# Performance work log

Measured on AMD Instinct MI355X. Metric: run time of the kernel, lower is better.

The kernel has to match this reference:

```python
import jax, jax.numpy as jnp
import numpy as np

V, E, H, L, B, T = 32000, 256, 512, 2, 64, 2048


def setup_inputs() -> dict:
    key = jax.random.key(0)
    ks = jax.random.split(key, 24)
    def rn(i, shape, scale=0.05):
        return jax.random.normal(ks[i], shape, jnp.float32) * scale
    inp = {
        "token": jax.random.randint(ks[0], (B,), 0, V),
        "h0": rn(1, (L, B, H), 1.0),
        "c0": rn(2, (L, B, H), 1.0),
        "encoder_outputs": rn(3, (B, T, H), 1.0),
        "mask": jax.random.randint(ks[4], (B, T), 0, 2).astype(jnp.int32),
        # parameters
        "emb_table": rn(5, (V, E), 1.0).at[0].set(0.0),  # padding_idx=0
        "W_attn": rn(6, (H, 2 * H)),
        "b_attn": rn(7, (H,)),
        "v_attn": jax.random.uniform(ks[8], (H,), jnp.float32),  # torch.rand init
        "W_ih0": rn(9, (4 * H, E + H)),
        "W_hh0": rn(10, (4 * H, H)),
        "b_ih0": rn(11, (4 * H,)),
        "b_hh0": rn(12, (4 * H,)),
        "W_ih1": rn(13, (4 * H, H)),
        "W_hh1": rn(14, (4 * H, H)),
        "b_ih1": rn(15, (4 * H,)),
        "b_hh1": rn(16, (4 * H,)),
        "W_out": rn(17, (V, H)),
        "b_out": rn(18, (V,)),
    }
    return inp


def _lstm_step(x, h, c, Wi, Wh, bi, bh):
    # PyTorch gate order: i, f, g, o
    gates = x @ Wi.T + bi + h @ Wh.T + bh  # [B, 4H]
    i, f, g, o = jnp.split(gates, 4, axis=-1)
    c_new = jax.nn.sigmoid(f) * c + jax.nn.sigmoid(i) * jnp.tanh(g)
    h_new = jax.nn.sigmoid(o) * jnp.tanh(c_new)
    return h_new, c_new


def reference(token, h0, c0, encoder_outputs, mask,
              emb_table, W_attn, b_attn, v_attn,
              W_ih0, W_hh0, b_ih0, b_hh0,
              W_ih1, W_hh1, b_ih1, b_hh1,
              W_out, b_out):
    embedded = emb_table[token]  # [B, E]

    # Bahdanau attention using the top-layer hidden state.
    # Linear on concat(hidden, enc) split into two matmuls (no T-tiling of hidden).
    h_top = h0[-1]  # [B, H]
    h_part = h_top @ W_attn[:, :H].T  # [B, H]
    e_part = jnp.einsum('bth,kh->btk', encoder_outputs, W_attn[:, H:])  # [B, T, H]
    energy = jnp.tanh(h_part[:, None, :] + e_part + b_attn) @ v_attn  # [B, T]
    energy = jnp.where(mask == 0, -jnp.inf, energy)
    attn_weights = jax.nn.softmax(energy, axis=1)  # [B, T]

    context = jnp.einsum('bt,bth->bh', attn_weights, encoder_outputs)  # [B, H]

    # Single-step 2-layer LSTM (eval mode: no inter-layer dropout).
    x0 = jnp.concatenate([embedded, context], axis=-1)  # [B, E+H]
    h0_new, c0_new = _lstm_step(x0, h0[0], c0[0], W_ih0, W_hh0, b_ih0, b_hh0)
    h1_new, c1_new = _lstm_step(h0_new, h0[1], c0[1], W_ih1, W_hh1, b_ih1, b_hh1)

    logits = h1_new @ W_out.T + b_out  # [B, V]
    h_new = jnp.stack([h0_new, h1_new])  # [L, B, H]
    c_new = jnp.stack([c0_new, c1_new])
    return logits, (h_new, c_new), attn_weights
```

## Files before the change

### kernel.cpp

```cpp
#include <hip/hip_runtime.h>
#include <hip/hip_fp16.h>
#include <cmath>

typedef _Float16 f16x8 __attribute__((ext_vector_type(8)));
typedef _Float16 f16x4 __attribute__((ext_vector_type(4)));
typedef float f32x4 __attribute__((ext_vector_type(4)));

#define NV 32000
#define NE 256
#define NH 512
#define NB 64
#define NT 2048

__device__ __forceinline__ float fast_tanh(float x) {
  return 1.f - 2.f / (__expf(2.f * x) + 1.f);
}
__device__ __forceinline__ float fast_sig(float x) {
  return 1.f / (1.f + __expf(-x));
}

__global__ void k_swz_be(const float* __restrict__ Wattn, _Float16* __restrict__ Be) {
  int idx = blockIdx.x * 256 + threadIdx.x;
  int l = idx & 63, nt = (idx >> 6) & 31, kc = idx >> 11;
  int n = (nt << 4) + (l & 15);
  int h0 = (kc << 5) + ((l >> 4) << 3);
  const float* s = Wattn + n * 1024 + 512 + h0;
  _Float16* d = Be + idx * 8;
  #pragma unroll
  for (int j = 0; j < 8; ++j) d[j] = (_Float16)s[j];
}

__global__ void k_prep_htop(const float* __restrict__ h0, _Float16* __restrict__ xh,
                            _Float16* __restrict__ xcat1) {
  int b = blockIdx.x, t = threadIdx.x;
  _Float16 v = (_Float16)h0[NB * NH + b * NH + t];
  xh[b * NH + t] = v;
  xcat1[b * 1024 + 512 + t] = v;
}

template <int KLEN>
__global__ __launch_bounds__(128)
void k_gemm_bT(const _Float16* __restrict__ A, int K,
               const float* __restrict__ B0, int ldb0,
               const float* __restrict__ B1, int ldb1, int b1k,
               const float* __restrict__ bias,
               float* __restrict__ out, int N) {
  int ntiles = N >> 5;
  int bn = blockIdx.x % ntiles, kcid = blockIdx.x / ntiles;
  int tid = threadIdx.x, w = tid >> 6, l = tid & 63;
  int n = (bn << 5) + (w << 4) + (l & 15);
  int kq = (l >> 4) << 3;
  int k0 = kcid * KLEN;
  f32x4 acc[4];
  #pragma unroll
  for (int mi = 0; mi < 4; ++mi) acc[mi] = (f32x4){0.f, 0.f, 0.f, 0.f};
  #pragma unroll 2
  for (int kk = 0; kk < KLEN; kk += 32) {
    int kbase = k0 + kk;
    f16x8 a[4];
    #pragma unroll
    for (int mi = 0; mi < 4; ++mi)
      a[mi] = *(const f16x8*)(A + (size_t)((l & 15) + (mi << 4)) * K + kbase + kq);
    const float* bp;
    if (B1 && kbase >= b1k) bp = B1 + (size_t)n * ldb1 + (kbase - b1k) + kq;
    else                    bp = B0 + (size_t)n * ldb0 + kbase + kq;
    float4 x0 = *(const float4*)bp;
    float4 x1 = *(const float4*)(bp + 4);
    f16x8 bf = {(_Float16)x0.x, (_Float16)x0.y, (_Float16)x0.z, (_Float16)x0.w,
                (_Float16)x1.x, (_Float16)x1.y, (_Float16)x1.z, (_Float16)x1.w};
    #pragma unroll
    for (int mi = 0; mi < 4; ++mi)
      acc[mi] = __builtin_amdgcn_mfma_f32_16x16x32_f16(a[mi], bf, acc[mi], 0, 0, 0);
  }
  float* op = out + (size_t)kcid * 64 * N;
  #pragma unroll
  for (int mi = 0; mi < 4; ++mi)
    #pragma unroll
    for (int r = 0; r < 4; ++r) {
      int row = (mi << 4) + ((l >> 4) << 2) + r;
      float v = acc[mi][r];
      if (bias) v += bias[n];
      op[(size_t)row * N + n] = v;
    }
}

__global__ __launch_bounds__(512, 4)
void k_energy(const float* __restrict__ enc, const _Float16* __restrict__ Be,
              const float* __restrict__ hp0, const float* __restrict__ hp1,
              const float* __restrict__ battn, const float* __restrict__ vat,
              const int* __restrict__ mask,
              float* __restrict__ eng, float* __restrict__ mcsc,
              float* __restrict__ numpart) {
  __shared__ _Float16 As[64 * 512];
  __shared__ float hpl[NH], vl[NH], ep[64][8], wl[64];
  int tile = blockIdx.x;
  int b = tile >> 5;
  long row0 = (long)tile << 6;
  int tid = threadIdx.x;
  hpl[tid] = hp0[(b << 9) + tid] + hp1[(b << 9) + tid] + battn[tid];
  vl[tid] = vat[tid];
  int w = tid >> 6, l = tid & 63;

  const float4* encp = (const float4*)(enc + row0 * NH);
  for (int half = 0; half < 2; ++half) {
    float4 st[8];
    #pragma unroll
    for (int i = 0; i < 8; ++i) st[i] = encp[tid + ((half * 8 + i) << 9)];
    #pragma unroll
    for (int i = 0; i < 8; ++i) {
      int s = tid + ((half * 8 + i) << 9);
      int r = s >> 7, c4 = s & 127;
      f16x4 h4 = {(_Float16)st[i].x, (_Float16)st[i].y,
                  (_Float16)st[i].z, (_Float16)st[i].w};
      *(f16x4*)((char*)As + (r << 10) + (((c4 << 3)) ^ ((r & 7) << 4))) = h4;
    }
  }
  __syncthreads();

  f32x4 acc[4][4];
  #pragma unroll
  for (int mi = 0; mi < 4; ++mi)
    #pragma unroll
    for (int ni = 0; ni < 4; ++ni) acc[mi][ni] = (f32x4){0.f, 0.f, 0.f, 0.f};

  for (int kc = 0; kc < 16; ++kc) {
    f16x8 a[4], bf[4];
    int kb = (kc << 6) + ((l >> 4) << 4);
    #pragma unroll
    for (int mi = 0; mi < 4; ++mi) {
      int r = (mi << 4) + (l & 15);
      a[mi] = *(const f16x8*)((char*)As + (r << 10) + (kb ^ ((r & 7) << 4)));
    }
    #pragma unroll
    for (int ni = 0; ni < 4; ++ni)
      bf[ni] = *(const f16x8*)(Be + (size_t)((((kc << 5) + (w << 2) + ni) << 6) + l) * 8);
    #pragma unroll
    for (int mi = 0; mi < 4; ++mi)
      #pragma unroll
      for (int ni = 0; ni < 4; ++ni)
        acc[mi][ni] = __builtin_amdgcn_mfma_f32_16x16x32_f16(a[mi], bf[ni], acc[mi][ni], 0, 0, 0);
  }

  int cl = l & 15;
  #pragma unroll
  for (int mi = 0; mi < 4; ++mi) {
    float s0 = 0.f, s1 = 0.f, s2 = 0.f, s3 = 0.f;
    #pragma unroll
    for (int ni = 0; ni < 4; ++ni) {
      int col = (w << 6) + (ni << 4) + cl;
      float hv = hpl[col], vv = vl[col];
      s0 += vv * fast_tanh(acc[mi][ni][0] + hv);
      s1 += vv * fast_tanh(acc[mi][ni][1] + hv);
      s2 += vv * fast_tanh(acc[mi][ni][2] + hv);
      s3 += vv * fast_tanh(acc[mi][ni][3] + hv);
    }
    #pragma unroll
    for (int off = 1; off < 16; off <<= 1) {
      s0 += __shfl_xor(s0, off, 64);
      s1 += __shfl_xor(s1, off, 64);
      s2 += __shfl_xor(s2, off, 64);
      s3 += __shfl_xor(s3, off, 64);
    }
    if (cl == 0) {
      int rb = (mi << 4) + ((l >> 4) << 2);
      ep[rb][w] = s0; ep[rb + 1][w] = s1; ep[rb + 2][w] = s2; ep[rb + 3][w] = s3;
    }
  }
  __syncthreads();

  if (tid < 64) {
    float e = 0.f;
    #pragma unroll
    for (int q = 0; q < 8; ++q) e += ep[tid][q];
    int mk = mask[row0 + tid];
    e = mk ? e : -3.0e38f;
    eng[row0 + tid] = e;
    float m = e;
    #pragma unroll
    for (int off = 32; off; off >>= 1) m = fmaxf(m, __shfl_xor(m, off, 64));
    float wv = mk ? __expf(e - m) : 0.f;
    float s = wv;
    #pragma unroll
    for (int off = 32; off; off >>= 1) s += __shfl_xor(s, off, 64);
    wl[tid] = wv;
    if (tid == 0) { mcsc[tile * 2] = m; mcsc[tile * 2 + 1] = s; }
  }
  __syncthreads();

  float a = 0.f;
  #pragma unroll 4
  for (int t = 0; t < 64; ++t) {
    float ev = (float)(*(const _Float16*)((char*)As + (t << 10) + (((tid * 2)) ^ ((t & 7) << 4))));
    a += wl[t] * ev;
  }
  numpart[(size_t)tile * NH + tid] = a;
}

__global__ void k_combine(const float* __restrict__ mcsc, const float* __restrict__ numpart,
                          const float* __restrict__ eng, const int* __restrict__ token,
                          const float* __restrict__ emb, const float* __restrict__ h0,
                          _Float16* __restrict__ xcat0, float* __restrict__ attw) {
  __shared__ float scale_s[32], Ms, dens;
  int b = blockIdx.x, tid = threadIdx.x;
  if (tid < 32) {
    float m = mcsc[(b * 32 + tid) * 2];
    float s = mcsc[(b * 32 + tid) * 2 + 1];
    float M = m;
    #pragma unroll
    for (int off = 16; off; off >>= 1) M = fmaxf(M, __shfl_xor(M, off, 32));
    float sc = __expf(m - M);
    float d = sc * s;
    #pragma unroll
    for (int off = 16; off; off >>= 1) d += __shfl_xor(d, off, 32);
    scale_s[tid] = sc;
    if (tid == 0) { Ms = M; dens = d; }
  }
  __syncthreads();
  float M = Ms, rden = 1.f / dens;
  float a = 0.f;
  #pragma unroll 4
  for (int c = 0; c < 32; ++c) a += scale_s[c] * numpart[(size_t)(b * 32 + c) * NH + tid];
  xcat0[b * 1280 + 256 + tid] = (_Float16)(a * rden);
  if (tid < 256) xcat0[b * 1280 + tid] = (_Float16)emb[(size_t)token[b] * NE + tid];
  xcat0[b * 1280 + 768 + tid] = (_Float16)h0[b * NH + tid];
  #pragma unroll
  for (int i = 0; i < 4; ++i) {
    int t = tid + (i << 9);
    attw[(b << 11) + t] = __expf(eng[(b << 11) + t] - M) * rden;
  }
}

__global__ void k_act(const float* __restrict__ pg, const float* __restrict__ bih,
                      const float* __restrict__ bhh, const float* __restrict__ cprev,
                      float* __restrict__ hout, float* __restrict__ cout,
                      _Float16* __restrict__ hf16, int hpitch, int nchunks) {
  int idx = blockIdx.x * 256 + threadIdx.x;
  int b = idx >> 9, u = idx & 511;
  float g[4];
  #pragma unroll
  for (int gi = 0; gi < 4; ++gi) {
    float s = bih[gi * 512 + u] + bhh[gi * 512 + u];
    for (int kc = 0; kc < nchunks; ++kc)
      s += pg[((size_t)kc * 64 + b) * 2048 + gi * 512 + u];
    g[gi] = s;
  }
  float c = fast_sig(g[1]) * cprev[idx] + fast_sig(g[0]) * fast_tanh(g[2]);
  float h = fast_sig(g[3]) * fast_tanh(c);
  cout[idx] = c;
  hout[idx] = h;
  hf16[b * hpitch + u] = (_Float16)h;
}

extern "C" void kernel_launch(void* const* d_in, const int* in_sizes, int n_in,
                              void* d_out, int out_size, void* d_ws, size_t ws_size,
                              hipStream_t stream) {
  (void)in_sizes; (void)n_in; (void)out_size; (void)ws_size;
  const int*   token = (const int*)d_in[0];
  const float* h0    = (const float*)d_in[1];
  const float* c0    = (const float*)d_in[2];
  const float* enc   = (const float*)d_in[3];
  const int*   mask  = (const int*)d_in[4];
  const float* emb   = (const float*)d_in[5];
  const float* Wattn = (const float*)d_in[6];
  const float* battn = (const float*)d_in[7];
  const float* vattn = (const float*)d_in[8];
  const float* Wih0  = (const float*)d_in[9];
  const float* Whh0  = (const float*)d_in[10];
  const float* bih0  = (const float*)d_in[11];
  const float* bhh0  = (const float*)d_in[12];
  const float* Wih1  = (const float*)d_in[13];
  const float* Whh1  = (const float*)d_in[14];
  const float* bih1  = (const float*)d_in[15];
  const float* bhh1  = (const float*)d_in[16];
  const float* Wout  = (const float*)d_in[17];
  const float* bout  = (const float*)d_in[18];

  float* ws    = (float*)d_ws;
  float* pghp  = ws;
  float* eng   = pghp + 65536;
  float* mcsc  = eng + 131072;
  float* np    = mcsc + 4096;
  float* pg0   = np + 1048576;
  float* pg1   = pg0 + 524288;
  _Float16* Be    = (_Float16*)(pg1 + 524288);
  _Float16* xh    = Be + 262144;
  _Float16* xcat0 = xh + 32768;
  _Float16* xcat1 = xcat0 + 81920;
  _Float16* h1f   = xcat1 + 65536;

  float* out    = (float*)d_out;
  float* logits = out;
  float* hnew   = out + (size_t)NB * NV;
  float* cnew   = hnew + 2 * NB * NH;
  float* attw   = cnew + 2 * NB * NH;

  k_swz_be<<<dim3(128), dim3(256), 0, stream>>>(Wattn, Be);
  k_prep_htop<<<dim3(64), dim3(512), 0, stream>>>(h0, xh, xcat1);
  k_gemm_bT<256><<<dim3(32), dim3(128), 0, stream>>>(
      xh, NH, Wattn, 1024, nullptr, 0, 1 << 30, nullptr, pghp, NH);
  k_energy<<<dim3(2048), dim3(512), 0, stream>>>(
      enc, Be, pghp, pghp + 32768, battn, vattn, mask, eng, mcsc, np);
  k_combine<<<dim3(64), dim3(512), 0, stream>>>(
      mcsc, np, eng, token, emb, h0, xcat0, attw);
  k_gemm_bT<320><<<dim3(256), dim3(128), 0, stream>>>(
      xcat0, 1280, Wih0, 768, Whh0, NH, 768, nullptr, pg0, 2048);
  k_act<<<dim3(128), dim3(256), 0, stream>>>(
      pg0, bih0, bhh0, c0, hnew, cnew, xcat1, 1024, 4);
  k_gemm_bT<256><<<dim3(256), dim3(128), 0, stream>>>(
      xcat1, 1024, Wih1, NH, Whh1, NH, NH, nullptr, pg1, 2048);
  k_act<<<dim3(128), dim3(256), 0, stream>>>(
      pg1, bih1, bhh1, c0 + NB * NH, hnew + NB * NH, cnew + NB * NH, h1f, 512, 4);
  k_gemm_bT<512><<<dim3(1000), dim3(128), 0, stream>>>(
      h1f, NH, Wout, NH, nullptr, 0, 1 << 30, bout, logits, NV);
}
```

Before: 193.6 us.

## Overlap second-half encoder load with first-half MFMA and vectorize context reduction

The encoder tile is now staged into LDS in two K-halves. The global loads for the second half are issued before the first-half MFMA loop runs, so their latency is hidden behind compute. The per-tile softmax is computed redundantly by every wave, which drops one block barrier. The weighted context sum now reads f16x4 vectors across four row groups and combines them through a small LDS scratch buffer. This adds LDS usage and an extra reduction step, and the eight in-flight float4 registers per thread could raise register pressure.

```diff
diff --git a/kernel.cpp b/kernel.cpp
--- a/kernel.cpp
+++ b/kernel.cpp
@@ -84,6 +84,45 @@
     }
 }
 
+
+#define ISSUE8(rs, t, h)                                                       \
+  { const float4* gp = (const float4*)(enc + (size_t)(t) * 32768 + (h) * 256); \
+    _Pragma("unroll")                                                          \
+    for (int ii = 0; ii < 8; ++ii) {                                           \
+      int s_ = tid + ii * 512;                                                 \
+      rs[ii] = gp[(s_ >> 6) * 128 + (s_ & 63)];                                \
+    } }
+
+#define WRITE8(rs, h)                                                          \
+  { _Pragma("unroll")                                                          \
+    for (int ii = 0; ii < 8; ++ii) {                                           \
+      int s_ = tid + ii * 512;                                                 \
+      int r_ = s_ >> 6, c4_ = s_ & 63;                                         \
+      f16x4 h4_ = {(_Float16)rs[ii].x, (_Float16)rs[ii].y,                     \
+                   (_Float16)rs[ii].z, (_Float16)rs[ii].w};                    \
+      *(f16x4*)((char*)As + (r_ << 10) +                                       \
+                ((((h) << 9) + (c4_ << 3)) ^ ((r_ & 7) << 4))) = h4_;          \
+    } }
+
+#define MFMA_KC(klo, khi)                                                      \
+  for (int kc = (klo); kc < (khi); ++kc) {                                     \
+    f16x8 afr[4];                                                              \
+    _Pragma("unroll")                                                          \
+    for (int mi = 0; mi < 4; ++mi) {                                           \
+      int r_ = (mi << 4) + (l & 15);                                           \
+      afr[mi] = *(const f16x8*)((char*)As + (r_ << 10) +                       \
+                 (((kc << 6) + ((l >> 4) << 4)) ^ ((r_ & 7) << 4)));           \
+    }                                                                          \
+    _Pragma("unroll")                                                          \
+    for (int ni = 0; ni < 4; ++ni) {                                           \
+      f16x8 bfr = *(const f16x8*)(Be +                                         \
+          (size_t)((((kc << 5) + (w << 2) + ni) << 6) + l) * 8);               \
+      _Pragma("unroll")                                                        \
+      for (int mi = 0; mi < 4; ++mi)                                           \
+        acc[mi][ni] = __builtin_amdgcn_mfma_f32_16x16x32_f16(afr[mi], bfr,     \
+                                                             acc[mi][ni], 0, 0, 0); \
+    } }
+
 __global__ __launch_bounds__(512, 4)
 void k_energy(const float* __restrict__ enc, const _Float16* __restrict__ Be,
               const float* __restrict__ hp0, const float* __restrict__ hp1,
@@ -92,30 +131,18 @@
               float* __restrict__ eng, float* __restrict__ mcsc,
               float* __restrict__ numpart) {
   __shared__ _Float16 As[64 * 512];
-  __shared__ float hpl[NH], vl[NH], ep[64][8], wl[64];
+  __shared__ float hpl[NH], vl[NH], ep[64][8], wl[64], psc[4][NH];
   int tile = blockIdx.x;
   int b = tile >> 5;
   long row0 = (long)tile << 6;
-  int tid = threadIdx.x;
+  int tid = threadIdx.x, w = tid >> 6, l = tid & 63;
   hpl[tid] = hp0[(b << 9) + tid] + hp1[(b << 9) + tid] + battn[tid];
   vl[tid] = vat[tid];
-  int w = tid >> 6, l = tid & 63;
-
-  const float4* encp = (const float4*)(enc + row0 * NH);
-  for (int half = 0; half < 2; ++half) {
-    float4 st[8];
-    #pragma unroll
-    for (int i = 0; i < 8; ++i) st[i] = encp[tid + ((half * 8 + i) << 9)];
-    #pragma unroll
-    for (int i = 0; i < 8; ++i) {
-      int s = tid + ((half * 8 + i) << 9);
-      int r = s >> 7, c4 = s & 127;
-      f16x4 h4 = {(_Float16)st[i].x, (_Float16)st[i].y,
-                  (_Float16)st[i].z, (_Float16)st[i].w};
-      *(f16x4*)((char*)As + (r << 10) + (((c4 << 3)) ^ ((r & 7) << 4))) = h4;
-    }
-  }
-  __syncthreads();
+
+  float4 rs[8];
+  ISSUE8(rs, tile, 0);
+  WRITE8(rs, 0);
+  ISSUE8(rs, tile, 1);
 
   f32x4 acc[4][4];
   #pragma unroll
@@ -123,23 +150,11 @@
     #pragma unroll
     for (int ni = 0; ni < 4; ++ni) acc[mi][ni] = (f32x4){0.f, 0.f, 0.f, 0.f};
 
-  for (int kc = 0; kc < 16; ++kc) {
-    f16x8 a[4], bf[4];
-    int kb = (kc << 6) + ((l >> 4) << 4);
-    #pragma unroll
-    for (int mi = 0; mi < 4; ++mi) {
-      int r = (mi << 4) + (l & 15);
-      a[mi] = *(const f16x8*)((char*)As + (r << 10) + (kb ^ ((r & 7) << 4)));
-    }
-    #pragma unroll
-    for (int ni = 0; ni < 4; ++ni)
-      bf[ni] = *(const f16x8*)(Be + (size_t)((((kc << 5) + (w << 2) + ni) << 6) + l) * 8);
-    #pragma unroll
-    for (int mi = 0; mi < 4; ++mi)
-      #pragma unroll
-      for (int ni = 0; ni < 4; ++ni)
-        acc[mi][ni] = __builtin_amdgcn_mfma_f32_16x16x32_f16(a[mi], bf[ni], acc[mi][ni], 0, 0, 0);
-  }
+  __syncthreads();
+  MFMA_KC(0, 8);
+  WRITE8(rs, 1);
+  __syncthreads();
+  MFMA_KC(8, 16);
 
   int cl = l & 15;
   #pragma unroll
@@ -168,13 +183,13 @@
   }
   __syncthreads();
 
-  if (tid < 64) {
-    float e = 0.f;
-    #pragma unroll
-    for (int q = 0; q < 8; ++q) e += ep[tid][q];
-    int mk = mask[row0 + tid];
+  {
+    float4 e0 = *(const float4*)&ep[l][0];
+    float4 e1 = *(const float4*)&ep[l][4];
+    float e = (e0.x + e0.y) + (e0.z + e0.w) + (e1.x + e1.y) + (e1.z + e1.w);
+    int mk = mask[row0 + l];
     e = mk ? e : -3.0e38f;
-    eng[row0 + tid] = e;
+    if (w == 0) eng[row0 + l] = e;
     float m = e;
     #pragma unroll
     for (int off = 32; off; off >>= 1) m = fmaxf(m, __shfl_xor(m, off, 64));
@@ -182,18 +197,28 @@
     float s = wv;
     #pragma unroll
     for (int off = 32; off; off >>= 1) s += __shfl_xor(s, off, 64);
-    wl[tid] = wv;
+    wl[l] = wv;
     if (tid == 0) { mcsc[tile * 2] = m; mcsc[tile * 2 + 1] = s; }
   }
-  __syncthreads();
-
-  float a = 0.f;
-  #pragma unroll 4
-  for (int t = 0; t < 64; ++t) {
-    float ev = (float)(*(const _Float16*)((char*)As + (t << 10) + (((tid * 2)) ^ ((t & 7) << 4))));
-    a += wl[t] * ev;
-  }
-  numpart[(size_t)tile * NH + tid] = a;
+
+  {
+    int rg = tid >> 7, j4 = tid & 127;
+    float c0a = 0.f, c1a = 0.f, c2a = 0.f, c3a = 0.f;
+    #pragma unroll 4
+    for (int r16 = 0; r16 < 16; ++r16) {
+      int t = (rg << 4) + r16;
+      f16x4 hv = *(const f16x4*)((char*)As + (t << 10) +
+                                 ((j4 << 3) ^ ((t & 7) << 4)));
+      float wv = wl[t];
+      c0a += wv * (float)hv[0]; c1a += wv * (float)hv[1];
+      c2a += wv * (float)hv[2]; c3a += wv * (float)hv[3];
+    }
+    *(float4*)&psc[rg][j4 << 2] = (float4){c0a, c1a, c2a, c3a};
+  }
+  __syncthreads();
+
+  numpart[(size_t)tile * NH + tid] =
+      psc[0][tid] + psc[1][tid] + psc[2][tid] + psc[3][tid];
 }
 
 __global__ void k_combine(const float* __restrict__ mcsc, const float* __restrict__ numpart,
```

New measurement: 254.8 us. +31.6%, slower.

## Pipeline encoder loads into LDS asynchronously in a multi-tile energy kernel

Applied to the files above, without the earlier changes.

The energy kernel is restructured so each block handles 8 consecutive 64-row tiles rather than one, with the grid shrunk to 256 blocks. Encoder rows are streamed as fp32 straight into a 4-stage LDS ring via global_load_lds, using explicit vmcnt waits and barriers. Conversion to fp16 now happens while MFMA fragments are built, so global-memory latency overlaps with matrix work instead of sitting in a load-then-compute phase. The weighted context sum now re-reads the encoder tile from global memory (hoping for cache hits) instead of reusing an fp16 LDS copy. This raises LDS usage to about 140KB per block, which limits occupancy to one block per CU.

```diff
diff --git a/kernel.cpp b/kernel.cpp
--- a/kernel.cpp
+++ b/kernel.cpp
@@ -17,6 +17,10 @@
 }
 __device__ __forceinline__ float fast_sig(float x) {
   return 1.f / (1.f + __expf(-x));
+}
+__device__ __forceinline__ void gll16(const void* g, void* l) {
+  __builtin_amdgcn_global_load_lds((const __attribute__((address_space(1))) void*)g,
+                                   (__attribute__((address_space(3))) void*)l, 16, 0, 0);
 }
 
 __global__ void k_swz_be(const float* __restrict__ Wattn, _Float16* __restrict__ Be) {
@@ -84,116 +88,156 @@
     }
 }
 
-__global__ __launch_bounds__(512, 4)
+
+#define WAITVM(N) asm volatile("s_waitcnt vmcnt(" #N ")" ::: "memory")
+#define SBAR() { __builtin_amdgcn_sched_barrier(0); __builtin_amdgcn_s_barrier(); \
+                 __builtin_amdgcn_sched_barrier(0); }
+#define LBAR() { asm volatile("s_waitcnt lgkmcnt(0)" ::: "memory"); \
+                 __builtin_amdgcn_s_barrier(); __builtin_amdgcn_sched_barrier(0); }
+
+#define ISSUE(g)                                                               \
+  { int t_ = t0 + ((g) >> 2); int q_ = (g) & 3; float* bq_ = buf[q_];          \
+    _Pragma("unroll")                                                          \
+    for (int k_ = 0; k_ < 4; ++k_) {                                           \
+      int rw_ = (w << 3) + (k_ << 1) + (l >> 5);                               \
+      const char* gp_ = (const char*)enc + ((size_t)((t_ << 6) + rw_) << 11) + \
+                        (q_ << 9) + (((l & 31) << 4) ^ ((rw_ & 7) << 4));      \
+      gll16(gp_, (char*)&bq_[((w << 3) + (k_ << 1)) << 7]);                    \
+    } }
+
+__global__ __launch_bounds__(512, 2)
 void k_energy(const float* __restrict__ enc, const _Float16* __restrict__ Be,
               const float* __restrict__ hp0, const float* __restrict__ hp1,
               const float* __restrict__ battn, const float* __restrict__ vat,
               const int* __restrict__ mask,
               float* __restrict__ eng, float* __restrict__ mcsc,
               float* __restrict__ numpart) {
-  __shared__ _Float16 As[64 * 512];
-  __shared__ float hpl[NH], vl[NH], ep[64][8], wl[64];
-  int tile = blockIdx.x;
-  int b = tile >> 5;
-  long row0 = (long)tile << 6;
-  int tid = threadIdx.x;
+  __shared__ float buf[4][64 * 128];
+  __shared__ float hpl[NH], vl[NH], ep[64][8], wl[64], psc[4][NH];
+  __shared__ int ml[512];
+  int bid = blockIdx.x;
+  int tid = threadIdx.x, w = tid >> 6, l = tid & 63;
+  int b = bid >> 2;
+  int t0 = bid << 3;
+
   hpl[tid] = hp0[(b << 9) + tid] + hp1[(b << 9) + tid] + battn[tid];
   vl[tid] = vat[tid];
-  int w = tid >> 6, l = tid & 63;
-
-  const float4* encp = (const float4*)(enc + row0 * NH);
-  for (int half = 0; half < 2; ++half) {
-    float4 st[8];
-    #pragma unroll
-    for (int i = 0; i < 8; ++i) st[i] = encp[tid + ((half * 8 + i) << 9)];
-    #pragma unroll
-    for (int i = 0; i < 8; ++i) {
-      int s = tid + ((half * 8 + i) << 9);
-      int r = s >> 7, c4 = s & 127;
-      f16x4 h4 = {(_Float16)st[i].x, (_Float16)st[i].y,
-                  (_Float16)st[i].z, (_Float16)st[i].w};
-      *(f16x4*)((char*)As + (r << 10) + (((c4 << 3)) ^ ((r & 7) << 4))) = h4;
-    }
-  }
-  __syncthreads();
-
-  f32x4 acc[4][4];
-  #pragma unroll
-  for (int mi = 0; mi < 4; ++mi)
-    #pragma unroll
-    for (int ni = 0; ni < 4; ++ni) acc[mi][ni] = (f32x4){0.f, 0.f, 0.f, 0.f};
-
-  for (int kc = 0; kc < 16; ++kc) {
-    f16x8 a[4], bf[4];
-    int kb = (kc << 6) + ((l >> 4) << 4);
+  ml[tid] = mask[((size_t)t0 << 6) + tid];
+
+  ISSUE(0); ISSUE(1); ISSUE(2);
+
+  for (int j = 0; j < 8; ++j) {
+    int tile = t0 + j;
+    long row0 = (long)tile << 6;
+    f32x4 acc[4][4];
+    #pragma unroll
+    for (int mi = 0; mi < 4; ++mi)
+      #pragma unroll
+      for (int ni = 0; ni < 4; ++ni) acc[mi][ni] = (f32x4){0.f, 0.f, 0.f, 0.f};
+
+    for (int q = 0; q < 4; ++q) {
+      int g = (j << 2) + q;
+      if (g + 3 < 32) { ISSUE(g + 3); }
+      int rem = 31 - g;
+      if (rem >= 3)      WAITVM(12);
+      else if (rem == 2) WAITVM(8);
+      else if (rem == 1) WAITVM(4);
+      else               WAITVM(0);
+      LBAR();
+
+      const float* bq = buf[q];
+      #pragma unroll
+      for (int kcl = 0; kcl < 4; ++kcl) {
+        int kcg = (q << 2) + kcl;
+        f16x8 afr[4];
+        #pragma unroll
+        for (int mi = 0; mi < 4; ++mi) {
+          int r_ = (mi << 4) + (l & 15);
+          const char* rowp = (const char*)(bq + (r_ << 7));
+          int b0 = (kcl << 7) + ((l >> 4) << 5);
+          int sw = (r_ & 7) << 4;
+          f32x4 lo = *(const f32x4*)(rowp + (b0 ^ sw));
+          f32x4 hi = *(const f32x4*)(rowp + ((b0 + 16) ^ sw));
+          afr[mi] = (f16x8){(_Float16)lo[0], (_Float16)lo[1],
+                            (_Float16)lo[2], (_Float16)lo[3],
+                            (_Float16)hi[0], (_Float16)hi[1],
+                            (_Float16)hi[2], (_Float16)hi[3]};
+        }
+        #pragma unroll
+        for (int ni = 0; ni < 4; ++ni) {
+          f16x8 bfr = *(const f16x8*)(Be +
+              (size_t)((((kcg << 5) + (w << 2) + ni) << 6) + l) * 8);
+          #pragma unroll
+          for (int mi = 0; mi < 4; ++mi)
+            acc[mi][ni] = __builtin_amdgcn_mfma_f32_16x16x32_f16(
+                afr[mi], bfr, acc[mi][ni], 0, 0, 0);
+        }
+      }
+      SBAR();
+    }
+
+    int cl = l & 15;
     #pragma unroll
     for (int mi = 0; mi < 4; ++mi) {
-      int r = (mi << 4) + (l & 15);
-      a[mi] = *(const f16x8*)((char*)As + (r << 10) + (kb ^ ((r & 7) << 4)));
-    }
-    #pragma unroll
-    for (int ni = 0; ni < 4; ++ni)
-      bf[ni] = *(const f16x8*)(Be + (size_t)((((kc << 5) + (w << 2) + ni) << 6) + l) * 8);
-    #pragma unroll
-    for (int mi = 0; mi < 4; ++mi)
-      #pragma unroll
-      for (int ni = 0; ni < 4; ++ni)
-        acc[mi][ni] = __builtin_amdgcn_mfma_f32_16x16x32_f16(a[mi], bf[ni], acc[mi][ni], 0, 0, 0);
-  }
-
-  int cl = l & 15;
-  #pragma unroll
-  for (int mi = 0; mi < 4; ++mi) {
-    float s0 = 0.f, s1 = 0.f, s2 = 0.f, s3 = 0.f;
-    #pragma unroll
-    for (int ni = 0; ni < 4; ++ni) {
-      int col = (w << 6) + (ni << 4) + cl;
-      float hv = hpl[col], vv = vl[col];
-      s0 += vv * fast_tanh(acc[mi][ni][0] + hv);
-      s1 += vv * fast_tanh(acc[mi][ni][1] + hv);
-      s2 += vv * fast_tanh(acc[mi][ni][2] + hv);
-      s3 += vv * fast_tanh(acc[mi][ni][3] + hv);
-    }
-    #pragma unroll
-    for (int off = 1; off < 16; off <<= 1) {
-      s0 += __shfl_xor(s0, off, 64);
-      s1 += __shfl_xor(s1, off, 64);
-      s2 += __shfl_xor(s2, off, 64);
-      s3 += __shfl_xor(s3, off, 64);
-    }
-    if (cl == 0) {
-      int rb = (mi << 4) + ((l >> 4) << 2);
-      ep[rb][w] = s0; ep[rb + 1][w] = s1; ep[rb + 2][w] = s2; ep[rb + 3][w] = s3;
-    }
-  }
-  __syncthreads();
-
-  if (tid < 64) {
-    float e = 0.f;
-    #pragma unroll
-    for (int q = 0; q < 8; ++q) e += ep[tid][q];
-    int mk = mask[row0 + tid];
-    e = mk ? e : -3.0e38f;
-    eng[row0 + tid] = e;
-    float m = e;
-    #pragma unroll
-    for (int off = 32; off; off >>= 1) m = fmaxf(m, __shfl_xor(m, off, 64));
-    float wv = mk ? __expf(e - m) : 0.f;
-    float s = wv;
-    #pragma unroll
-    for (int off = 32; off; off >>= 1) s += __shfl_xor(s, off, 64);
-    wl[tid] = wv;
-    if (tid == 0) { mcsc[tile * 2] = m; mcsc[tile * 2 + 1] = s; }
-  }
-  __syncthreads();
-
-  float a = 0.f;
-  #pragma unroll 4
-  for (int t = 0; t < 64; ++t) {
-    float ev = (float)(*(const _Float16*)((char*)As + (t << 10) + (((tid * 2)) ^ ((t & 7) << 4))));
-    a += wl[t] * ev;
-  }
-  numpart[(size_t)tile * NH + tid] = a;
+      float s0 = 0.f, s1 = 0.f, s2 = 0.f, s3 = 0.f;
+      #pragma unroll
+      for (int ni = 0; ni < 4; ++ni) {
+        int col = (w << 6) + (ni << 4) + cl;
+        float hv = hpl[col], vv = vl[col];
+        s0 += vv * fast_tanh(acc[mi][ni][0] + hv);
+        s1 += vv * fast_tanh(acc[mi][ni][1] + hv);
+        s2 += vv * fast_tanh(acc[mi][ni][2] + hv);
+        s3 += vv * fast_tanh(acc[mi][ni][3] + hv);
+      }
+      #pragma unroll
+      for (int off = 1; off < 16; off <<= 1) {
+        s0 += __shfl_xor(s0, off, 64);
+        s1 += __shfl_xor(s1, off, 64);
+        s2 += __shfl_xor(s2, off, 64);
+        s3 += __shfl_xor(s3, off, 64);
+      }
+      if (cl == 0) {
+        int rb = (mi << 4) + ((l >> 4) << 2);
+        ep[rb][w] = s0; ep[rb + 1][w] = s1; ep[rb + 2][w] = s2; ep[rb + 3][w] = s3;
+      }
+    }
+    LBAR();
+
+    {
+      float4 e0 = *(const float4*)&ep[l][0];
+      float4 e1 = *(const float4*)&ep[l][4];
+      float e = (e0.x + e0.y) + (e0.z + e0.w) + (e1.x + e1.y) + (e1.z + e1.w);
+      int mk = ml[(j << 6) + l];
+      e = mk ? e : -3.0e38f;
+      if (w == 0) eng[row0 + l] = e;
+      float m = e;
+      #pragma unroll
+      for (int off = 32; off; off >>= 1) m = fmaxf(m, __shfl_xor(m, off, 64));
+      float wv = mk ? __expf(e - m) : 0.f;
+      float s = wv;
+      #pragma unroll
+      for (int off = 32; off; off >>= 1) s += __shfl_xor(s, off, 64);
+      wl[l] = wv;
+      if (tid == 0) { mcsc[tile * 2] = m; mcsc[tile * 2 + 1] = s; }
+    }
+
+    {
+      int rg = tid >> 7, j4 = tid & 127;
+      const float* gp = enc + (((size_t)tile << 6) + ((size_t)rg << 4)) * NH + (j4 << 2);
+      float c0a = 0.f, c1a = 0.f, c2a = 0.f, c3a = 0.f;
+      #pragma unroll 4
+      for (int r16 = 0; r16 < 16; ++r16) {
+        float4 ev = *(const float4*)(gp + (size_t)r16 * NH);
+        float wv = wl[(rg << 4) + r16];
+        c0a += wv * ev.x; c1a += wv * ev.y; c2a += wv * ev.z; c3a += wv * ev.w;
+      }
+      *(float4*)&psc[rg][j4 << 2] = (float4){c0a, c1a, c2a, c3a};
+    }
+    LBAR();
+
+    numpart[(size_t)tile * NH + tid] =
+        psc[0][tid] + psc[1][tid] + psc[2][tid] + psc[3][tid];
+  }
 }
 
 __global__ void k_combine(const float* __restrict__ mcsc, const float* __restrict__ numpart,
@@ -298,7 +342,7 @@
   k_prep_htop<<<dim3(64), dim3(512), 0, stream>>>(h0, xh, xcat1);
   k_gemm_bT<256><<<dim3(32), dim3(128), 0, stream>>>(
       xh, NH, Wattn, 1024, nullptr, 0, 1 << 30, nullptr, pghp, NH);
-  k_energy<<<dim3(2048), dim3(512), 0, stream>>>(
+  k_energy<<<dim3(256), dim3(512), 0, stream>>>(
       enc, Be, pghp, pghp + 32768, battn, vattn, mask, eng, mcsc, np);
   k_combine<<<dim3(64), dim3(512), 0, stream>>>(
       mcsc, np, eng, token, emb, h0, xcat0, attw);
```

Result: slower. 280.1 us (+44.7%).

## Halve energy tile to 32 rows and overlap second K-half load with MFMA

Applied to the files above, without the earlier changes.

The attention-energy kernel now works on 32-row tiles with 256 threads, launching twice as many blocks. It loads the first half of the encoder columns, then prefetches the second half into registers while the MFMA loop runs on the first half. Each wave now covers 128 output columns, and the context partial sum uses f16x4 vector LDS reads. Partial numerators double in size, which adds workspace traffic and a longer reduction loop in k_combine. The bias and v vectors are stored in LDS as fp16, which adds a small rounding error.

```diff
diff --git a/kernel.cpp b/kernel.cpp
--- a/kernel.cpp
+++ b/kernel.cpp
@@ -84,71 +84,111 @@
     }
 }
 
-__global__ __launch_bounds__(512, 4)
+__global__ __launch_bounds__(256, 4)
 void k_energy(const float* __restrict__ enc, const _Float16* __restrict__ Be,
               const float* __restrict__ hp0, const float* __restrict__ hp1,
               const float* __restrict__ battn, const float* __restrict__ vat,
               const int* __restrict__ mask,
               float* __restrict__ eng, float* __restrict__ mcsc,
               float* __restrict__ numpart) {
-  __shared__ _Float16 As[64 * 512];
-  __shared__ float hpl[NH], vl[NH], ep[64][8], wl[64];
+  __shared__ _Float16 As[32 * 512];
+  __shared__ _Float16 hplh[NH], vlh[NH];
+  __shared__ float ep[32][4], wl[32], psc[2][NH];
   int tile = blockIdx.x;
-  int b = tile >> 5;
-  long row0 = (long)tile << 6;
-  int tid = threadIdx.x;
-  hpl[tid] = hp0[(b << 9) + tid] + hp1[(b << 9) + tid] + battn[tid];
-  vl[tid] = vat[tid];
-  int w = tid >> 6, l = tid & 63;
+  int b = tile >> 6;
+  long row0 = (long)tile << 5;
+  int tid = threadIdx.x, w = tid >> 6, l = tid & 63;
+  #pragma unroll
+  for (int i = 0; i < 2; ++i) {
+    int c = tid + (i << 8);
+    hplh[c] = (_Float16)(hp0[(b << 9) + c] + hp1[(b << 9) + c] + battn[c]);
+    vlh[c] = (_Float16)vat[c];
+  }
 
   const float4* encp = (const float4*)(enc + row0 * NH);
-  for (int half = 0; half < 2; ++half) {
-    float4 st[8];
-    #pragma unroll
-    for (int i = 0; i < 8; ++i) st[i] = encp[tid + ((half * 8 + i) << 9)];
-    #pragma unroll
-    for (int i = 0; i < 8; ++i) {
-      int s = tid + ((half * 8 + i) << 9);
-      int r = s >> 7, c4 = s & 127;
-      f16x4 h4 = {(_Float16)st[i].x, (_Float16)st[i].y,
-                  (_Float16)st[i].z, (_Float16)st[i].w};
-      *(f16x4*)((char*)As + (r << 10) + (((c4 << 3)) ^ ((r & 7) << 4))) = h4;
-    }
-  }
-  __syncthreads();
-
-  f32x4 acc[4][4];
-  #pragma unroll
-  for (int mi = 0; mi < 4; ++mi)
-    #pragma unroll
-    for (int ni = 0; ni < 4; ++ni) acc[mi][ni] = (f32x4){0.f, 0.f, 0.f, 0.f};
-
-  for (int kc = 0; kc < 16; ++kc) {
-    f16x8 a[4], bf[4];
-    int kb = (kc << 6) + ((l >> 4) << 4);
-    #pragma unroll
-    for (int mi = 0; mi < 4; ++mi) {
+  float4 rs[8];
+  #pragma unroll
+  for (int i = 0; i < 8; ++i) {
+    int s = tid + (i << 8);
+    rs[i] = encp[(s >> 6) * 128 + (s & 63)];
+  }
+  #pragma unroll
+  for (int i = 0; i < 8; ++i) {
+    int s = tid + (i << 8);
+    int r = s >> 6, c4 = s & 63;
+    f16x4 h4 = {(_Float16)rs[i].x, (_Float16)rs[i].y,
+                (_Float16)rs[i].z, (_Float16)rs[i].w};
+    *(f16x4*)((char*)As + (r << 10) + ((c4 << 3) ^ ((r & 7) << 4))) = h4;
+  }
+  #pragma unroll
+  for (int i = 0; i < 8; ++i) {
+    int s = tid + (i << 8);
+    rs[i] = encp[(s >> 6) * 128 + 64 + (s & 63)];
+  }
+
+  f32x4 acc[2][8];
+  #pragma unroll
+  for (int mi = 0; mi < 2; ++mi)
+    #pragma unroll
+    for (int ni = 0; ni < 8; ++ni) acc[mi][ni] = (f32x4){0.f, 0.f, 0.f, 0.f};
+
+  __syncthreads();
+  #pragma unroll
+  for (int kc = 0; kc < 8; ++kc) {
+    f16x8 afr[2];
+    #pragma unroll
+    for (int mi = 0; mi < 2; ++mi) {
       int r = (mi << 4) + (l & 15);
-      a[mi] = *(const f16x8*)((char*)As + (r << 10) + (kb ^ ((r & 7) << 4)));
-    }
-    #pragma unroll
-    for (int ni = 0; ni < 4; ++ni)
-      bf[ni] = *(const f16x8*)(Be + (size_t)((((kc << 5) + (w << 2) + ni) << 6) + l) * 8);
-    #pragma unroll
-    for (int mi = 0; mi < 4; ++mi)
+      afr[mi] = *(const f16x8*)((char*)As + (r << 10) +
+                 (((kc << 6) + ((l >> 4) << 4)) ^ ((r & 7) << 4)));
+    }
+    #pragma unroll
+    for (int ni = 0; ni < 8; ++ni) {
+      f16x8 bfr = *(const f16x8*)(Be +
+          (size_t)((((kc << 5) + (w << 3) + ni) << 6) + l) * 8);
       #pragma unroll
-      for (int ni = 0; ni < 4; ++ni)
-        acc[mi][ni] = __builtin_amdgcn_mfma_f32_16x16x32_f16(a[mi], bf[ni], acc[mi][ni], 0, 0, 0);
+      for (int mi = 0; mi < 2; ++mi)
+        acc[mi][ni] = __builtin_amdgcn_mfma_f32_16x16x32_f16(afr[mi], bfr,
+                                                             acc[mi][ni], 0, 0, 0);
+    }
+  }
+  #pragma unroll
+  for (int i = 0; i < 8; ++i) {
+    int s = tid + (i << 8);
+    int r = s >> 6, c4 = s & 63;
+    f16x4 h4 = {(_Float16)rs[i].x, (_Float16)rs[i].y,
+                (_Float16)rs[i].z, (_Float16)rs[i].w};
+    *(f16x4*)((char*)As + (r << 10) + ((512 + (c4 << 3)) ^ ((r & 7) << 4))) = h4;
+  }
+  __syncthreads();
+  #pragma unroll
+  for (int kc = 8; kc < 16; ++kc) {
+    f16x8 afr[2];
+    #pragma unroll
+    for (int mi = 0; mi < 2; ++mi) {
+      int r = (mi << 4) + (l & 15);
+      afr[mi] = *(const f16x8*)((char*)As + (r << 10) +
+                 (((kc << 6) + ((l >> 4) << 4)) ^ ((r & 7) << 4)));
+    }
+    #pragma unroll
+    for (int ni = 0; ni < 8; ++ni) {
+      f16x8 bfr = *(const f16x8*)(Be +
+          (size_t)((((kc << 5) + (w << 3) + ni) << 6) + l) * 8);
+      #pragma unroll
+      for (int mi = 0; mi < 2; ++mi)
+        acc[mi][ni] = __builtin_amdgcn_mfma_f32_16x16x32_f16(afr[mi], bfr,
+                                                             acc[mi][ni], 0, 0, 0);
+    }
   }
 
   int cl = l & 15;
   #pragma unroll
-  for (int mi = 0; mi < 4; ++mi) {
+  for (int mi = 0; mi < 2; ++mi) {
     float s0 = 0.f, s1 = 0.f, s2 = 0.f, s3 = 0.f;
     #pragma unroll
-    for (int ni = 0; ni < 4; ++ni) {
-      int col = (w << 6) + (ni << 4) + cl;
-      float hv = hpl[col], vv = vl[col];
+    for (int ni = 0; ni < 8; ++ni) {
+      int col = (w << 7) + (ni << 4) + cl;
+      float hv = (float)hplh[col], vv = (float)vlh[col];
       s0 += vv * fast_tanh(acc[mi][ni][0] + hv);
       s1 += vv * fast_tanh(acc[mi][ni][1] + hv);
       s2 += vv * fast_tanh(acc[mi][ni][2] + hv);
@@ -168,58 +208,68 @@
   }
   __syncthreads();
 
-  if (tid < 64) {
-    float e = 0.f;
-    #pragma unroll
-    for (int q = 0; q < 8; ++q) e += ep[tid][q];
-    int mk = mask[row0 + tid];
+  {
+    int r = l & 31;
+    float4 e4 = *(const float4*)&ep[r][0];
+    float e = (e4.x + e4.y) + (e4.z + e4.w);
+    int mk = mask[row0 + r];
     e = mk ? e : -3.0e38f;
-    eng[row0 + tid] = e;
+    if (tid < 32) eng[row0 + tid] = e;
     float m = e;
     #pragma unroll
-    for (int off = 32; off; off >>= 1) m = fmaxf(m, __shfl_xor(m, off, 64));
+    for (int off = 16; off; off >>= 1) m = fmaxf(m, __shfl_xor(m, off, 64));
     float wv = mk ? __expf(e - m) : 0.f;
     float s = wv;
     #pragma unroll
-    for (int off = 32; off; off >>= 1) s += __shfl_xor(s, off, 64);
-    wl[tid] = wv;
+    for (int off = 16; off; off >>= 1) s += __shfl_xor(s, off, 64);
+    wl[r] = wv;
     if (tid == 0) { mcsc[tile * 2] = m; mcsc[tile * 2 + 1] = s; }
   }
-  __syncthreads();
-
-  float a = 0.f;
-  #pragma unroll 4
-  for (int t = 0; t < 64; ++t) {
-    float ev = (float)(*(const _Float16*)((char*)As + (t << 10) + (((tid * 2)) ^ ((t & 7) << 4))));
-    a += wl[t] * ev;
-  }
-  numpart[(size_t)tile * NH + tid] = a;
+
+  {
+    int rg = tid >> 7, j4 = tid & 127;
+    float c0a = 0.f, c1a = 0.f, c2a = 0.f, c3a = 0.f;
+    #pragma unroll 4
+    for (int r16 = 0; r16 < 16; ++r16) {
+      int t = (rg << 4) + r16;
+      f16x4 hv = *(const f16x4*)((char*)As + (t << 10) +
+                                 ((j4 << 3) ^ ((t & 7) << 4)));
+      float wv = wl[t];
+      c0a += wv * (float)hv[0]; c1a += wv * (float)hv[1];
+      c2a += wv * (float)hv[2]; c3a += wv * (float)hv[3];
+    }
+    *(float4*)&psc[rg][j4 << 2] = (float4){c0a, c1a, c2a, c3a};
+  }
+  __syncthreads();
+
+  numpart[(size_t)tile * NH + tid]       = psc[0][tid] + psc[1][tid];
+  numpart[(size_t)tile * NH + 256 + tid] = psc[0][256 + tid] + psc[1][256 + tid];
 }
 
 __global__ void k_combine(const float* __restrict__ mcsc, const float* __restrict__ numpart,
                           const float* __restrict__ eng, const int* __restrict__ token,
                           const float* __restrict__ emb, const float* __restrict__ h0,
                           _Float16* __restrict__ xcat0, float* __restrict__ attw) {
-  __shared__ float scale_s[32], Ms, dens;
+  __shared__ float scale_s[64], Ms, dens;
   int b = blockIdx.x, tid = threadIdx.x;
-  if (tid < 32) {
-    float m = mcsc[(b * 32 + tid) * 2];
-    float s = mcsc[(b * 32 + tid) * 2 + 1];
+  if (tid < 64) {
+    float m = mcsc[(b * 64 + tid) * 2];
+    float s = mcsc[(b * 64 + tid) * 2 + 1];
     float M = m;
     #pragma unroll
-    for (int off = 16; off; off >>= 1) M = fmaxf(M, __shfl_xor(M, off, 32));
+    for (int off = 32; off; off >>= 1) M = fmaxf(M, __shfl_xor(M, off, 64));
     float sc = __expf(m - M);
     float d = sc * s;
     #pragma unroll
-    for (int off = 16; off; off >>= 1) d += __shfl_xor(d, off, 32);
+    for (int off = 32; off; off >>= 1) d += __shfl_xor(d, off, 64);
     scale_s[tid] = sc;
     if (tid == 0) { Ms = M; dens = d; }
   }
   __syncthreads();
   float M = Ms, rden = 1.f / dens;
   float a = 0.f;
-  #pragma unroll 4
-  for (int c = 0; c < 32; ++c) a += scale_s[c] * numpart[(size_t)(b * 32 + c) * NH + tid];
+  #pragma unroll 8
+  for (int c = 0; c < 64; ++c) a += scale_s[c] * numpart[(size_t)(b * 64 + c) * NH + tid];
   xcat0[b * 1280 + 256 + tid] = (_Float16)(a * rden);
   if (tid < 256) xcat0[b * 1280 + tid] = (_Float16)emb[(size_t)token[b] * NE + tid];
   xcat0[b * 1280 + 768 + tid] = (_Float16)h0[b * NH + tid];
@@ -279,8 +329,8 @@
   float* pghp  = ws;
   float* eng   = pghp + 65536;
   float* mcsc  = eng + 131072;
-  float* np    = mcsc + 4096;
-  float* pg0   = np + 1048576;
+  float* np    = mcsc + 8192;
+  float* pg0   = np + 2097152;
   float* pg1   = pg0 + 524288;
   _Float16* Be    = (_Float16*)(pg1 + 524288);
   _Float16* xh    = Be + 262144;
@@ -298,7 +348,7 @@
   k_prep_htop<<<dim3(64), dim3(512), 0, stream>>>(h0, xh, xcat1);
   k_gemm_bT<256><<<dim3(32), dim3(128), 0, stream>>>(
       xh, NH, Wattn, 1024, nullptr, 0, 1 << 30, nullptr, pghp, NH);
-  k_energy<<<dim3(2048), dim3(512), 0, stream>>>(
+  k_energy<<<dim3(4096), dim3(256), 0, stream>>>(
       enc, Be, pghp, pghp + 32768, battn, vattn, mask, eng, mcsc, np);
   k_combine<<<dim3(64), dim3(512), 0, stream>>>(
       mcsc, np, eng, token, emb, h0, xcat0, attw);
```

Result: slower. 265.4 us (+37.1%).
